# Performance work log

Measured on AMD Instinct MI355X. Metric: run time of the kernel, lower is better.

Reference implementation:

```python
import jax, jax.numpy as jnp
import numpy as np

D_MODEL = 256; N_HEADS = 8; D_FF = 1024; N_LAYERS = 8; N_BLOCKS = 4
VOCAB = 10000; N_SPARSE = 26; N_DENSE = 13; BATCH = 4096
SEQ = N_DENSE + N_SPARSE  # 39 feature tokens


def _ln(x, g, b, eps=1e-5):
    m = jnp.mean(x, -1, keepdims=True)
    v = jnp.mean((x - m) ** 2, -1, keepdims=True)
    return (x - m) * jax.lax.rsqrt(v + eps) * g + b


def _normalize(x, axis=-1, eps=1e-12):
    n = jnp.maximum(jnp.linalg.norm(x, axis=axis, keepdims=True), eps)
    return x / n


def setup_inputs() -> dict:
    key = jax.random.key(0)
    ks = iter(jax.random.split(key, 64))
    d, L, ff = D_MODEL, N_LAYERS, D_FF
    w = lambda shape: jax.random.normal(next(ks), shape, dtype=jnp.float32) * 0.02
    z = lambda shape: jnp.zeros(shape, jnp.float32)
    o = lambda shape: jnp.ones(shape, jnp.float32)
    return {
        "dense_x": jax.random.normal(next(ks), (BATCH, N_DENSE), dtype=jnp.float32),
        "sparse_x": jax.random.randint(next(ks), (BATCH, N_SPARSE), 0, VOCAB, dtype=jnp.int32),
        "W_dense": w((N_DENSE * d, N_DENSE)), "b_dense": z((N_DENSE * d,)),
        "emb": w((N_SPARSE, VOCAB + 1, d)),
        "Wq": w((L, d, d)), "bq": z((L, d)),
        "Wk": w((L, d, d)), "bk": z((L, d)),
        "Wv": w((L, d, d)), "bv": z((L, d)),
        "W1": w((L, ff, d)), "b1": z((L, ff)),
        "W2": w((L, d, ff)), "b2": z((L, d)),
        "n1g": o((L, d)), "n1b": z((L, d)),
        "n2g": o((L, d)), "n2b": z((L, d)),
        "qvec": w((N_BLOCKS, d)),
        "mha_in_w": w((3 * d, d)), "mha_in_b": z((3 * d,)),
        "mha_out_w": w((d, d)), "mha_out_b": z((d,)),
        "ng": o((d,)), "ngb": z((d,)),
        "Wo1": w((D_FF, SEQ * d)), "bo1": z((D_FF,)),
        "Wo2": w((1, D_FF)), "bo2": z((1,)),
    }


def reference(dense_x, sparse_x, W_dense, b_dense, emb, Wq, bq, Wk, bk, Wv, bv,
              W1, b1, W2, b2, n1g, n1b, n2g, n2b, qvec,
              mha_in_w, mha_in_b, mha_out_w, mha_out_b, ng, ngb,
              Wo1, bo1, Wo2, bo2):
    B = dense_x.shape[0]; d = D_MODEL; H = N_HEADS; dh = d // H
    # --- embed_features ---
    dense_emb = (dense_x @ W_dense.T + b_dense).reshape(B, N_DENSE, d)
    emb0 = emb.at[:, 0, :].set(0.0)  # padding_idx=0
    sp = emb0[jnp.arange(N_SPARSE), sparse_x]  # [B, 26, d]
    x = jnp.concatenate([dense_emb, sp], axis=1)  # [B, 39, d]

    scale = 1.0 / jnp.sqrt(jnp.float32(d))  # note: d_model, not head_dim
    block_size = N_LAYERS // N_BLOCKS
    block_outputs = [x]
    for i in range(N_LAYERS):
        # --- HSTU layer: sigmoid pointwise attention ---
        r = x
        h = _ln(x, n1g[i], n1b[i])
        q = (h @ Wq[i].T + bq[i]).reshape(B, SEQ, H, dh).transpose(0, 2, 1, 3)
        k = (h @ Wk[i].T + bk[i]).reshape(B, SEQ, H, dh).transpose(0, 2, 1, 3)
        v = (h @ Wv[i].T + bv[i]).reshape(B, SEQ, H, dh).transpose(0, 2, 1, 3)
        aw = jax.nn.sigmoid(jnp.einsum('bhqd,bhkd->bhqk', q, k) * scale)
        ao = jnp.einsum('bhqk,bhkd->bhqd', aw, v).transpose(0, 2, 1, 3).reshape(B, SEQ, d)
        x = r + ao
        r = x
        h = _ln(x, n2g[i], n2b[i])
        x = r + (jax.nn.relu(h @ W1[i].T + b1[i]) @ W2[i].T + b2[i])
        # --- AttentionResidual block mixing ---
        if (i + 1) % block_size == 0 and i < N_LAYERS - 1:
            V = jnp.stack(block_outputs + [x])  # [n, B, T, d]
            K = _normalize(V)
            qi = min(len(block_outputs), N_BLOCKS - 1)
            qn = _normalize(qvec[qi], axis=0)
            logits = jnp.einsum('d,nbtd->nbt', qn, K)
            wt = jax.nn.softmax(logits, axis=0)
            x = jnp.einsum('nbt,nbtd->btd', wt, V)
            block_outputs.append(x)

    # --- final LayerNorm + standard MHA residual ---
    r = x
    h = _ln(x, ng, ngb)
    qkv = h @ mha_in_w.T + mha_in_b
    q, k, v = jnp.split(qkv, 3, axis=-1)
    q = q.reshape(B, SEQ, H, dh).transpose(0, 2, 1, 3)
    k = k.reshape(B, SEQ, H, dh).transpose(0, 2, 1, 3)
    v = v.reshape(B, SEQ, H, dh).transpose(0, 2, 1, 3)
    at = jax.nn.softmax(jnp.einsum('bhqd,bhkd->bhqk', q, k) / jnp.sqrt(jnp.float32(dh)), axis=-1)
    mo = jnp.einsum('bhqk,bhkd->bhqd', at, v).transpose(0, 2, 1, 3).reshape(B, SEQ, d)
    x = r + (mo @ mha_out_w.T + mha_out_b)

    flat = x.reshape(B, -1)
    return (jax.nn.relu(flat @ Wo1.T + bo1) @ Wo2.T + bo2).squeeze(-1)
```

## Files before the change

kernel.cpp:

```cpp
#include <hip/hip_runtime.h>
#include <hip/hip_bf16.h>

typedef __attribute__((ext_vector_type(4))) float f32x4;
typedef __attribute__((ext_vector_type(8))) short short8;
typedef __attribute__((ext_vector_type(4))) unsigned short us4;

static __device__ __forceinline__ unsigned short f2bf(float f){
  return __builtin_bit_cast(unsigned short, __float2bfloat16(f));
}
static __device__ __forceinline__ float bf2f(unsigned short u){
  return __bfloat162float(__builtin_bit_cast(__hip_bfloat16, u));
}
static __device__ __forceinline__ short8 zero8(){
  short8 v;
#pragma unroll
  for (int e=0;e<8;++e) v[e]=0;
  return v;
}
static __device__ __forceinline__ void g2l16(const void* g, void* l){
  __builtin_amdgcn_global_load_lds(
    (const __attribute__((address_space(1))) unsigned int*)g,
    (__attribute__((address_space(3))) unsigned int*)l, 16, 0, 0);
}

__global__ __launch_bounds__(256)
void qkv_k(const unsigned short* __restrict__ Ap,
           const unsigned short* __restrict__ Bp,
           const float* __restrict__ bias,
           unsigned short* __restrict__ qk,
           unsigned short* __restrict__ vT)
{
  __shared__ __align__(16) unsigned short As[128*256];

  const int tid = threadIdx.x, lane = tid & 63, w = tid >> 6;
  const int cl = lane & 15, q4 = lane >> 4;
  const long rowBase = (long)blockIdx.x << 7;
  const int wm = (w >> 1) << 6, wn = (w & 1) << 6;

#pragma unroll
  for (int it=0; it<16; ++it){
    const int c = (it<<8) + (w<<6) + lane;
    const int kt = c>>10, rem = c & 1023, r = rem>>3, x = rem&7;
    g2l16(Ap + (rowBase + r)*256 + (kt<<6) + (((x ^ (r&7)))<<3),
          As + (((it<<8) + (w<<6))<<3));
  }
  __syncthreads();

  for (int cb=0; cb<6; ++cb){
    f32x4 acc[4][4];
#pragma unroll
    for (int m=0;m<4;++m)
#pragma unroll
      for (int n=0;n<4;++n) acc[m][n] = (f32x4){0.f,0.f,0.f,0.f};
#pragma unroll
    for (int kt=0; kt<4; ++kt)
#pragma unroll
      for (int ks=0; ks<2; ++ks){
        const int kb = ks*64 + (q4<<4);
        short8 af[4], bf_[4];
#pragma unroll
        for (int m=0;m<4;++m){
          const int r = wm + m*16 + cl;
          af[m] = *(const short8*)((const char*)As + (kt<<14) + r*128 + (kb ^ ((r&7)<<4)));
        }
#pragma unroll
        for (int n=0;n<4;++n){
          const long rn = cb*128 + wn + n*16 + cl;
          bf_[n] = *(const short8*)(Bp + rn*256 + (kt<<6) + ks*32 + (q4<<3));
        }
#pragma unroll
        for (int m=0;m<4;++m)
#pragma unroll
          for (int n=0;n<4;++n)
            acc[m][n] = __builtin_amdgcn_mfma_f32_16x16x32_bf16(af[m], bf_[n], acc[m][n], 0,0,0);
      }
#pragma unroll
    for (int n=0;n<4;++n){
      const int col = cb*128 + wn + n*16 + cl;
      const float bi = bias[col];
#pragma unroll
      for (int m=0;m<4;++m){
        const long r0 = rowBase + wm + m*16 + (q4<<2);
#pragma unroll
        for (int i=0;i<4;++i){
          const float v = acc[m][n][i] + bi;
          const long row = r0 + i;
          if (col < 512){
            qk[row*512 + col] = f2bf(v);
          } else {
            const int bb = (int)row / 39;
            const int tt = (int)row - bb*39;
            unsigned short* vrow = vT + ((long)bb*256 + (col - 512))*48;
            vrow[tt] = f2bf(v);
            if (tt < 9) vrow[tt + 39] = 0;
          }
        }
      }
    }
  }
}

__global__ __launch_bounds__(256)
void gemm_k(const unsigned short* __restrict__ Ap, int lda,
            const unsigned short* __restrict__ Bp,
            const float* __restrict__ bias,
            unsigned short* __restrict__ Outp, int ldo, int K, int nColBlk)
{
  const int id = blockIdx.x;
  const int xcd = id & 7; const int t0 = id >> 3;
  const int cb = t0 % nColBlk; const int rb = (t0 / nColBlk)*8 + xcd;
  const long rowBase = (long)rb << 7;
  const long colBase = (long)cb << 7;
  const int tid = threadIdx.x, lane = tid & 63, w = tid >> 6;
  const int wm = (w >> 1) << 6, wn = (w & 1) << 6;
  const int cl = lane & 15, q4 = lane >> 4;

  __shared__ __align__(16) unsigned short As[128*64];
  __shared__ __align__(16) unsigned short Bs[128*64];

  const char* bSrc[4]; unsigned short* bDst[4];
  const char* aSrc[4]; unsigned short* aDst[4];
#pragma unroll
  for (int g=0; g<4; ++g){
    const int c = (w<<8) + (g<<6) + lane;
    const int r = c>>3, x = c&7, c16 = x ^ (r&7);
    bSrc[g] = (const char*)(Bp + (colBase + r)*(long)K) + c16*16;
    bDst[g] = Bs + (((w<<2)+g)<<9);
    aSrc[g] = (const char*)(Ap + (rowBase + r)*(long)lda) + c16*16;
    aDst[g] = As + (((w<<2)+g)<<9);
  }

  f32x4 acc[4][4];
#pragma unroll
  for (int m=0;m<4;++m)
#pragma unroll
    for (int n=0;n<4;++n) acc[m][n] = (f32x4){0.f,0.f,0.f,0.f};

  const int nk = K >> 6;
  for (int t=0; t<nk; ++t){
    if (t) __syncthreads();
    const long tb = (long)t << 7;
#pragma unroll
    for (int g=0; g<4; ++g){
      g2l16(bSrc[g] + tb, bDst[g]);
      g2l16(aSrc[g] + tb, aDst[g]);
    }
    __syncthreads();
#pragma unroll
    for (int ks=0; ks<2; ++ks){
      const int kb = ks*64 + (q4<<4);
      short8 af[4], bf_[4];
#pragma unroll
      for (int m=0;m<4;++m){
        const int r = wm + m*16 + cl;
        af[m] = *(const short8*)((const char*)As + r*128 + (kb ^ ((r&7)<<4)));
      }
#pragma unroll
      for (int n=0;n<4;++n){
        const int r = wn + n*16 + cl;
        bf_[n] = *(const short8*)((const char*)Bs + r*128 + (kb ^ ((r&7)<<4)));
      }
#pragma unroll
      for (int m=0;m<4;++m)
#pragma unroll
        for (int n=0;n<4;++n)
          acc[m][n] = __builtin_amdgcn_mfma_f32_16x16x32_bf16(af[m], bf_[n], acc[m][n], 0,0,0);
    }
  }

#pragma unroll
  for (int n=0;n<4;++n){
    const long col = colBase + wn + n*16 + cl;
    const float bi = bias[col];
#pragma unroll
    for (int m=0;m<4;++m){
      const long r0 = rowBase + wm + m*16 + (q4<<2);
#pragma unroll
      for (int i=0;i<4;++i){
        const float v = acc[m][n][i] + bi;
        Outp[(r0+i)*(long)ldo + col] = f2bf(fmaxf(v,0.f));
      }
    }
  }
}

__global__ __launch_bounds__(256, 2)
void ffn_k(const float* __restrict__ xf_in,
           const float* __restrict__ sB, const float* __restrict__ cB,
           const unsigned short* __restrict__ W1p,
           const float* __restrict__ b1p,
           const unsigned short* __restrict__ W2p,
           const float* __restrict__ b2p,
           float* __restrict__ xf,
           unsigned short* __restrict__ xln1)
{
  __shared__ __align__(16) unsigned short Wb1[64*256];
  __shared__ __align__(16) unsigned short Wb2[256*64];
  __shared__ __align__(16) unsigned short Hs[64*64];
  float* part1 = (float*)Wb1;
  float* part2 = part1 + 256;
  float* sln   = part2 + 256;
  float* cln   = sln + 64;

  const int tid = threadIdx.x, lane = tid & 63, w = tid >> 6;
  const int cl = lane & 15, q4 = lane >> 4;
  const long rowBase = (long)blockIdx.x << 6;

  short8 af[8];
  {
    const int row = (w<<4) + cl;
    const float s = sB[rowBase + row], c = cB[rowBase + row];
    const float* src = xf_in + (rowBase + row)*256 + (q4<<3);
#pragma unroll
    for (int kt=0; kt<8; ++kt){
      f32x4 a = *(const f32x4*)(src + kt*32);
      f32x4 b = *(const f32x4*)(src + kt*32 + 4);
      short8 v;
#pragma unroll
      for (int e=0;e<4;++e){ v[e] = (short)f2bf(a[e]*s + c); v[4+e] = (short)f2bf(b[e]*s + c); }
      af[kt] = v;
    }
  }

  f32x4 acc[4][4];
#pragma unroll
  for (int m=0;m<4;++m)
#pragma unroll
    for (int n=0;n<4;++n) acc[m][n] = (f32x4){0.f,0.f,0.f,0.f};

  for (int j=0; j<16; ++j){
    const int ffbase = j<<6;
    __syncthreads();
#pragma unroll
    for (int it=0; it<8; ++it){
      const int c = (it<<8) + tid;
      {
        const int kt = c>>9, cc = c&511, rr = cc>>3, xs = cc&7;
        g2l16(W1p + ((long)(ffbase+rr))*256 + (kt<<6) + ((xs^(rr&7))<<3),
              Wb1 + (((it<<8) + (w<<6))<<3));
      }
      {
        const int rr = c>>3, xs = c&7;
        g2l16(W2p + (long)rr*1024 + ffbase + ((xs^(rr&7))<<3),
              Wb2 + (((it<<8) + (w<<6))<<3));
      }
    }
    float b1v[4];
#pragma unroll
    for (int n=0;n<4;++n) b1v[n] = b1p[ffbase + n*16 + cl];
    __syncthreads();

    f32x4 hacc[4];
#pragma unroll
    for (int n=0;n<4;++n) hacc[n] = (f32x4){0.f,0.f,0.f,0.f};
#pragma unroll
    for (int kt2=0; kt2<4; ++kt2)
#pragma unroll
      for (int ks=0; ks<2; ++ks){
        const int kb = ks*64 + (q4<<4);
        const short8 a = af[kt2*2 + ks];
#pragma unroll
        for (int n=0;n<4;++n){
          const int rn = n*16 + cl;
          short8 bf_ = *(const short8*)((const char*)Wb1 + (kt2<<13) + rn*128 + (kb ^ ((rn&7)<<4)));
          hacc[n] = __builtin_amdgcn_mfma_f32_16x16x32_bf16(a, bf_, hacc[n], 0,0,0);
        }
      }
#pragma unroll
    for (int n=0;n<4;++n)
#pragma unroll
      for (int i=0;i<4;++i){
        const int hr = (w<<4) + (q4<<2) + i, hc = n*16 + cl;
        const float hv = fmaxf(hacc[n][i] + b1v[n], 0.f);
        *(unsigned short*)((char*)Hs + hr*128 + ((hc*2) ^ ((hr&7)<<4))) = f2bf(hv);
      }
    __syncthreads();

#pragma unroll
    for (int ks=0; ks<2; ++ks){
      const int kb = ks*64 + (q4<<4);
      short8 am[4], bm[4];
#pragma unroll
      for (int m=0;m<4;++m){
        const int r = m*16 + cl;
        am[m] = *(const short8*)((const char*)Hs + r*128 + (kb ^ ((r&7)<<4)));
      }
#pragma unroll
      for (int n=0;n<4;++n){
        const int r = (w<<6) + n*16 + cl;
        bm[n] = *(const short8*)((const char*)Wb2 + r*128 + (kb ^ ((r&7)<<4)));
      }
#pragma unroll
      for (int m=0;m<4;++m)
#pragma unroll
        for (int n=0;n<4;++n)
          acc[m][n] = __builtin_amdgcn_mfma_f32_16x16x32_bf16(am[m], bm[n], acc[m][n], 0,0,0);
    }
  }

#pragma unroll
  for (int n=0;n<4;++n){
    const int col = (w<<6) + n*16 + cl;
    const float bi = b2p[col];
#pragma unroll
    for (int m=0;m<4;++m)
#pragma unroll
      for (int i=0;i<4;++i){
        const int row = m*16 + (q4<<2) + i;
        const long gi = (rowBase + row)*256 + col;
        const float v = acc[m][n][i] + bi + xf[gi];
        acc[m][n][i] = v;
        xf[gi] = v;
      }
  }
  __syncthreads();
#pragma unroll
  for (int m=0;m<4;++m)
#pragma unroll
    for (int i=0;i<4;++i){
      float s1 = 0.f, s2 = 0.f;
#pragma unroll
      for (int n=0;n<4;++n){ const float v = acc[m][n][i]; s1 += v; s2 += v*v; }
#pragma unroll
      for (int off=8; off; off>>=1){ s1 += __shfl_xor(s1, off, 16); s2 += __shfl_xor(s2, off, 16); }
      const int row = m*16 + (q4<<2) + i;
      if (cl == 0){ part1[row*4 + w] = s1; part2[row*4 + w] = s2; }
    }
  __syncthreads();
  if (tid < 64){
    const float S1 = part1[tid*4]+part1[tid*4+1]+part1[tid*4+2]+part1[tid*4+3];
    const float S2 = part2[tid*4]+part2[tid*4+1]+part2[tid*4+2]+part2[tid*4+3];
    const float mn = S1*(1.f/256.f);
    const float var = S2*(1.f/256.f) - mn*mn;
    const float s = rsqrtf(var + 1e-5f);
    sln[tid] = s; cln[tid] = -mn*s;
  }
  __syncthreads();
#pragma unroll
  for (int m=0;m<4;++m)
#pragma unroll
    for (int i=0;i<4;++i){
      const int row = m*16 + (q4<<2) + i;
      const float s = sln[row], c = cln[row];
#pragma unroll
      for (int n=0;n<4;++n){
        const int col = (w<<6) + n*16 + cl;
        xln1[(rowBase + row)*256 + col] = f2bf(acc[m][n][i]*s + c);
      }
    }
}

__global__ __launch_bounds__(256)
void attn_sig_k(const unsigned short* __restrict__ qkb,
                const unsigned short* __restrict__ vT,
                float* xf, float* __restrict__ sB, float* __restrict__ cB)
{
  __shared__ __align__(16) unsigned short Ps[4*48*64];
  __shared__ float part[312];

  const int b = blockIdx.x;
  const int tid = threadIdx.x, lane = tid & 63, w = tid >> 6;
  const int cl = lane & 15, q4 = lane >> 4;
  unsigned short* P = Ps + w*3072;
  const unsigned short* qb = qkb + (long)b*39*512;
  const unsigned short* vbb = vT + (long)b*256*48;

  if (lane < 48){
    const int r = lane;
    *(short8*)((char*)P + r*128 + (96  ^ ((r&7)<<4))) = zero8();
    *(short8*)((char*)P + r*128 + (112 ^ ((r&7)<<4))) = zero8();
  }

  float ps1[3][4], ps2[3][4];
#pragma unroll
  for (int m=0;m<3;++m)
#pragma unroll
    for (int i=0;i<4;++i){ ps1[m][i]=0.f; ps2[m][i]=0.f; }

#pragma unroll
  for (int hh=0; hh<2; ++hh){
    const int h = (w<<1) + hh;
    f32x4 sac[3][3];
#pragma unroll
    for (int m=0;m<3;++m)
#pragma unroll
      for (int n=0;n<3;++n) sac[m][n] = (f32x4){0.f,0.f,0.f,0.f};
    short8 aq[3], bk8[3];
#pragma unroll
    for (int m=0;m<3;++m){
      const int r = m*16 + cl;
      aq[m] = (r < 39) ? *(const short8*)(qb + (long)r*512 + h*32 + q4*8) : zero8();
    }
#pragma unroll
    for (int n=0;n<3;++n){
      const int r = n*16 + cl;
      bk8[n] = (r < 39) ? *(const short8*)(qb + (long)r*512 + 256 + h*32 + q4*8) : zero8();
    }
#pragma unroll
    for (int m=0;m<3;++m)
#pragma unroll
      for (int n=0;n<3;++n)
        sac[m][n] = __builtin_amdgcn_mfma_f32_16x16x32_bf16(aq[m], bk8[n], sac[m][n], 0,0,0);
#pragma unroll
    for (int m=0;m<3;++m)
#pragma unroll
      for (int n=0;n<3;++n)
#pragma unroll
        for (int i=0;i<4;++i){
          const int row = m*16 + (q4<<2) + i, col = n*16 + cl;
          const float pv = 1.f/(1.f + __expf(-sac[m][n][i]*0.0625f));
          *(unsigned short*)((char*)P + row*128 + ((col*2) ^ ((row&7)<<4))) = f2bf(pv);
        }
    f32x4 aoc[3][2];
#pragma unroll
    for (int m=0;m<3;++m)
#pragma unroll
      for (int n=0;n<2;++n) aoc[m][n] = (f32x4){0.f,0.f,0.f,0.f};
#pragma unroll
    for (int ks=0; ks<2; ++ks){
      const int kb = ks*64 + (q4<<4);
      short8 pa[3], vb[2];
#pragma unroll
      for (int m=0;m<3;++m){
        const int r = m*16 + cl;
        pa[m] = *(const short8*)((const char*)P + r*128 + (kb ^ ((r&7)<<4)));
      }
#pragma unroll
      for (int n=0;n<2;++n){
        vb[n] = zero8();
        if (ks == 0 || q4 < 2)
          vb[n] = *(const short8*)(vbb + (long)(h*32 + n*16 + cl)*48 + ks*32 + q4*8);
      }
#pragma unroll
      for (int m=0;m<3;++m)
#pragma unroll
        for (int n=0;n<2;++n)
          aoc[m][n] = __builtin_amdgcn_mfma_f32_16x16x32_bf16(pa[m], vb[n], aoc[m][n], 0,0,0);
    }
#pragma unroll
    for (int m=0;m<3;++m)
#pragma unroll
      for (int n=0;n<2;++n)
#pragma unroll
        for (int i=0;i<4;++i){
          const int row = m*16 + (q4<<2) + i;
          if (row < 39){
            const long gi = (((long)(b*39+row))<<8) + h*32 + n*16 + cl;
            const float nv = xf[gi] + aoc[m][n][i];
            xf[gi] = nv;
            ps1[m][i] += nv; ps2[m][i] += nv*nv;
          }
        }
  }
#pragma unroll
  for (int m=0;m<3;++m)
#pragma unroll
    for (int i=0;i<4;++i){
      float a1 = ps1[m][i], a2 = ps2[m][i];
#pragma unroll
      for (int off=8; off; off>>=1){ a1 += __shfl_xor(a1, off, 16); a2 += __shfl_xor(a2, off, 16); }
      const int row = m*16 + (q4<<2) + i;
      if (cl == 0 && row < 39){ part[row*8 + (w<<1)] = a1; part[row*8 + (w<<1) + 1] = a2; }
    }
  __syncthreads();
  if (tid < 39){
    const float S1 = part[tid*8]+part[tid*8+2]+part[tid*8+4]+part[tid*8+6];
    const float S2 = part[tid*8+1]+part[tid*8+3]+part[tid*8+5]+part[tid*8+7];
    const float mn = S1*(1.f/256.f);
    const float var = S2*(1.f/256.f) - mn*mn;
    const float s = rsqrtf(var + 1e-5f);
    sB[b*39+tid] = s; cB[b*39+tid] = -mn*s;
  }
}

__global__ __launch_bounds__(256)
void attn_fin_k(const unsigned short* __restrict__ qkb,
                const unsigned short* __restrict__ vT,
                const float* __restrict__ xf,
                const unsigned short* __restrict__ moW,
                const float* __restrict__ moB,
                unsigned short* __restrict__ flatb)
{
  __shared__ __align__(16) unsigned short Ps[4*48*64];
  __shared__ __align__(16) unsigned short Mo[48*256];

  const int b = blockIdx.x;
  const int tid = threadIdx.x, lane = tid & 63, w = tid >> 6;
  const int cl = lane & 15, q4 = lane >> 4;
  unsigned short* P = Ps + w*3072;
  const unsigned short* qb = qkb + (long)b*39*512;
  const unsigned short* vbb = vT + (long)b*256*48;
  const float SC = 0.17677669529663687f;

  if (lane < 48){
    const int r = lane;
    *(short8*)((char*)P + r*128 + (96  ^ ((r&7)<<4))) = zero8();
    *(short8*)((char*)P + r*128 + (112 ^ ((r&7)<<4))) = zero8();
  }

#pragma unroll
  for (int hh=0; hh<2; ++hh){
    const int h = (w<<1) + hh;
    f32x4 sac[3][3];
#pragma unroll
    for (int m=0;m<3;++m)
#pragma unroll
      for (int n=0;n<3;++n) sac[m][n] = (f32x4){0.f,0.f,0.f,0.f};
    short8 aq[3], bk8[3];
#pragma unroll
    for (int m=0;m<3;++m){
      const int r = m*16 + cl;
      aq[m] = (r < 39) ? *(const short8*)(qb + (long)r*512 + h*32 + q4*8) : zero8();
    }
#pragma unroll
    for (int n=0;n<3;++n){
      const int r = n*16 + cl;
      bk8[n] = (r < 39) ? *(const short8*)(qb + (long)r*512 + 256 + h*32 + q4*8) : zero8();
    }
#pragma unroll
    for (int m=0;m<3;++m)
#pragma unroll
      for (int n=0;n<3;++n)
        sac[m][n] = __builtin_amdgcn_mfma_f32_16x16x32_bf16(aq[m], bk8[n], sac[m][n], 0,0,0);
#pragma unroll
    for (int m=0;m<3;++m)
#pragma unroll
      for (int i=0;i<4;++i){
        const float v0 = sac[m][0][i]*SC, v1 = sac[m][1][i]*SC, v2 = sac[m][2][i]*SC;
        const bool c2ok = (32 + cl) < 39;
        float mx = fmaxf(v0, v1);
        if (c2ok) mx = fmaxf(mx, v2);
#pragma unroll
        for (int off=8; off; off>>=1) mx = fmaxf(mx, __shfl_xor(mx, off, 16));
        const float e0 = __expf(v0-mx), e1 = __expf(v1-mx);
        const float e2 = c2ok ? __expf(v2-mx) : 0.f;
        float s = e0+e1+e2;
#pragma unroll
        for (int off=8; off; off>>=1) s += __shfl_xor(s, off, 16);
        const float inv = 1.f/s;
        const int row = m*16 + (q4<<2) + i;
        *(unsigned short*)((char*)P + row*128 + (((cl   )*2) ^ ((row&7)<<4))) = f2bf(e0*inv);
        *(unsigned short*)((char*)P + row*128 + (((16+cl)*2) ^ ((row&7)<<4))) = f2bf(e1*inv);
        *(unsigned short*)((char*)P + row*128 + (((32+cl)*2) ^ ((row&7)<<4))) = f2bf(e2*inv);
      }
    f32x4 aoc[3][2];
#pragma unroll
    for (int m=0;m<3;++m)
#pragma unroll
      for (int n=0;n<2;++n) aoc[m][n] = (f32x4){0.f,0.f,0.f,0.f};
#pragma unroll
    for (int ks=0; ks<2; ++ks){
      const int kb = ks*64 + (q4<<4);
      short8 pa[3], vb[2];
#pragma unroll
      for (int m=0;m<3;++m){
        const int r = m*16 + cl;
        pa[m] = *(const short8*)((const char*)P + r*128 + (kb ^ ((r&7)<<4)));
      }
#pragma unroll
      for (int n=0;n<2;++n){
        vb[n] = zero8();
        if (ks == 0 || q4 < 2)
          vb[n] = *(const short8*)(vbb + (long)(h*32 + n*16 + cl)*48 + ks*32 + q4*8);
      }
#pragma unroll
      for (int m=0;m<3;++m)
#pragma unroll
        for (int n=0;n<2;++n)
          aoc[m][n] = __builtin_amdgcn_mfma_f32_16x16x32_bf16(pa[m], vb[n], aoc[m][n], 0,0,0);
    }
#pragma unroll
    for (int m=0;m<3;++m)
#pragma unroll
      for (int n=0;n<2;++n)
#pragma unroll
        for (int i=0;i<4;++i){
          const int row = m*16 + (q4<<2) + i;
          const int colq = h*32 + n*16 + cl;
          *(unsigned short*)((char*)Mo + row*512 + ((colq*2) ^ ((row&7)<<4))) = f2bf(aoc[m][n][i]);
        }
  }
  __syncthreads();
  f32x4 oc[3][4];
#pragma unroll
  for (int m=0;m<3;++m)
#pragma unroll
    for (int n=0;n<4;++n) oc[m][n] = (f32x4){0.f,0.f,0.f,0.f};
#pragma unroll
  for (int ks=0; ks<8; ++ks){
    const int kb = ks*64 + (q4<<4);
    short8 am[3], bm[4];
#pragma unroll
    for (int m=0;m<3;++m){
      const int r = m*16 + cl;
      am[m] = *(const short8*)((const char*)Mo + r*512 + (kb ^ ((r&7)<<4)));
    }
#pragma unroll
    for (int n=0;n<4;++n){
      const int nn = (w<<6) + n*16 + cl;
      bm[n] = *(const short8*)(moW + (long)nn*256 + ks*32 + q4*8);
    }
#pragma unroll
    for (int m=0;m<3;++m)
#pragma unroll
      for (int n=0;n<4;++n)
        oc[m][n] = __builtin_amdgcn_mfma_f32_16x16x32_bf16(am[m], bm[n], oc[m][n], 0,0,0);
  }
#pragma unroll
  for (int m=0;m<3;++m)
#pragma unroll
    for (int n=0;n<4;++n)
#pragma unroll
      for (int i=0;i<4;++i){
        const int row = m*16 + (q4<<2) + i;
        if (row < 39){
          const int col = (w<<6) + n*16 + cl;
          const float v = oc[m][n][i] + moB[col] + xf[(((long)(b*39+row))<<8) + col];
          flatb[(long)b*9984 + row*256 + col] = f2bf(v);
        }
      }
}

__global__ __launch_bounds__(256)
void embed_k(const float* __restrict__ dense_x, const int* __restrict__ sparse_x,
             const float* __restrict__ W_dense, const float* __restrict__ b_dense,
             const float* __restrict__ emb,
             float* __restrict__ xf, unsigned short* __restrict__ x0b,
             unsigned short* __restrict__ xln1)
{
  const int bid = blockIdx.x;
  const int b = bid / 39, t = bid - b*39;
  const int c = threadIdx.x;
  float v;
  if (t < 13){
    const int j = t*256 + c;
    v = b_dense[j];
    const float* wr = W_dense + (long)j*13;
    const float* dx = dense_x + (long)b*13;
#pragma unroll
    for (int k2=0;k2<13;++k2) v = fmaf(dx[k2], wr[k2], v);
  } else {
    const int idx = sparse_x[b*26 + (t-13)];
    v = (idx == 0) ? 0.f : emb[((long)(t-13)*10001 + idx)*256 + c];
  }
  const long row = bid;
  xf[row*256 + c] = v;
  x0b[row*256 + c] = f2bf(v);
  float s1 = v, s2 = v*v;
#pragma unroll
  for (int off=32; off; off>>=1){ s1 += __shfl_xor(s1, off); s2 += __shfl_xor(s2, off); }
  __shared__ float r1[4], r2[4];
  const int lane = c & 63, wq = c >> 6;
  if (lane == 0){ r1[wq]=s1; r2[wq]=s2; }
  __syncthreads();
  const float S1 = r1[0]+r1[1]+r1[2]+r1[3];
  const float S2 = r2[0]+r2[1]+r2[2]+r2[3];
  const float mn = S1*(1.f/256.f);
  const float var = S2*(1.f/256.f) - mn*mn;
  const float s = rsqrtf(var+1e-5f);
  xln1[row*256 + c] = f2bf((v - mn)*s);
}

template<int NSRC>
__global__ __launch_bounds__(256)
void mix_k(float* __restrict__ xf,
           const unsigned short* __restrict__ s0,
           const unsigned short* __restrict__ s1p,
           const unsigned short* __restrict__ s2p,
           unsigned short* mout,
           const float* __restrict__ qvec, int qi,
           unsigned short* __restrict__ xln1)
{
  const int b = blockIdx.x;
  const int tid = threadIdx.x, lane = tid&63, w = tid>>6;
  const int c4 = lane << 2;
  f32x4 q = *(const f32x4*)(qvec + qi*256 + c4);
  float qq = q[0]*q[0]+q[1]*q[1]+q[2]*q[2]+q[3]*q[3];
#pragma unroll
  for (int off=32; off; off>>=1) qq += __shfl_xor(qq, off);
  const float qsc = 1.f/fmaxf(sqrtf(qq), 1e-12f);
#pragma unroll
  for (int e=0;e<4;++e) q[e] *= qsc;
  for (int t = w; t < 39; t += 4){
    const long ro = ((long)(b*39+t))*256 + c4;
    f32x4 v[NSRC];
#pragma unroll
    for (int n=0;n<NSRC;++n){
      if (n == NSRC-1) v[n] = *(const f32x4*)(xf + ro);
      else {
        const unsigned short* sp = (n==0)?s0:((n==1)?s1p:s2p);
        us4 u = *(const us4*)(sp + ro);
#pragma unroll
        for (int e=0;e<4;++e) v[n][e] = bf2f(u[e]);
      }
    }
    float lg[NSRC];
#pragma unroll
    for (int n=0;n<NSRC;++n){
      float nn = v[n][0]*v[n][0]+v[n][1]*v[n][1]+v[n][2]*v[n][2]+v[n][3]*v[n][3];
      float dd = q[0]*v[n][0]+q[1]*v[n][1]+q[2]*v[n][2]+q[3]*v[n][3];
#pragma unroll
      for (int off=32; off; off>>=1){ nn += __shfl_xor(nn,off); dd += __shfl_xor(dd,off); }
      lg[n] = dd / fmaxf(sqrtf(nn), 1e-12f);
    }
    float mx = lg[0];
#pragma unroll
    for (int n=1;n<NSRC;++n) mx = fmaxf(mx, lg[n]);
    float es = 0.f, e_[NSRC];
#pragma unroll
    for (int n=0;n<NSRC;++n){ e_[n] = __expf(lg[n]-mx); es += e_[n]; }
    const float inv = 1.f/es;
    f32x4 o = {0.f,0.f,0.f,0.f};
#pragma unroll
    for (int n=0;n<NSRC;++n){
      const float wt = e_[n]*inv;
#pragma unroll
      for (int e=0;e<4;++e) o[e] = fmaf(wt, v[n][e], o[e]);
    }
    *(f32x4*)(xf + ro) = o;
    if (mout){
      us4 u;
#pragma unroll
      for (int e=0;e<4;++e) u[e] = f2bf(o[e]);
      *(us4*)(mout + ro) = u;
    }
    float s1 = o[0]+o[1]+o[2]+o[3];
    float s2 = o[0]*o[0]+o[1]*o[1]+o[2]*o[2]+o[3]*o[3];
#pragma unroll
    for (int off=32; off; off>>=1){ s1 += __shfl_xor(s1,off); s2 += __shfl_xor(s2,off); }
    const float mn = s1*(1.f/256.f);
    const float var = s2*(1.f/256.f)-mn*mn;
    const float s = rsqrtf(var+1e-5f);
    const float c = -mn*s;
    us4 u2;
#pragma unroll
    for (int e=0;e<4;++e) u2[e] = f2bf(o[e]*s + c);
    *(us4*)(xln1 + ro) = u2;
  }
}

__global__ __launch_bounds__(256)
void head2_k(const unsigned short* __restrict__ h1h, const float* __restrict__ Wo2,
             const float* __restrict__ bo2, float* __restrict__ outp)
{
  const int b = blockIdx.x*4 + (threadIdx.x>>6);
  const int lane = threadIdx.x & 63;
  float s = 0.f;
#pragma unroll
  for (int g=0; g<2; ++g){
    const int base = lane*16 + g*8;
    short8 v8 = *(const short8*)(h1h + (long)b*1024 + base);
#pragma unroll
    for (int e=0;e<8;++e) s = fmaf(bf2f((unsigned short)v8[e]), Wo2[base+e], s);
  }
#pragma unroll
  for (int off=32; off; off>>=1) s += __shfl_xor(s, off);
  if (lane==0) outp[b] = s + bo2[0];
}

__global__ void cvt_k(const float* __restrict__ src, unsigned short* __restrict__ dst, long n){
  const long i = (long)blockIdx.x*256 + threadIdx.x;
  if (i < n) dst[i] = f2bf(src[i]);
}
__global__ void prep_qkv_k(const float* Wq, const float* Wk, const float* Wv,
                           const float* g, unsigned short* dst){
  const int n = blockIdx.x, i = blockIdx.y, k = threadIdx.x;
  const int sel = n >> 8, nn = n & 255;
  const float* W = sel==0?Wq:(sel==1?Wk:Wv);
  dst[((long)i*768 + n)*256 + k] = f2bf(W[((long)i*256+nn)*256 + k] * g[i*256+k]);
}
__global__ void prep_qkvb_k(const float* Wq,const float* Wk,const float* Wv,
                            const float* bq,const float* bk,const float* bv,
                            const float* beta, float* dst){
  const int n = blockIdx.x, i = blockIdx.y, k = threadIdx.x;
  const int sel = n>>8, nn = n&255;
  const float* W = sel==0?Wq:(sel==1?Wk:Wv);
  const float* bb = sel==0?bq:(sel==1?bk:bv);
  float v = beta[i*256+k] * W[((long)i*256+nn)*256+k];
  __shared__ float r[4];
#pragma unroll
  for (int off=32; off; off>>=1) v += __shfl_xor(v, off);
  if ((k&63)==0) r[k>>6] = v;
  __syncthreads();
  if (k==0) dst[i*768+n] = bb[i*256+nn] + r[0]+r[1]+r[2]+r[3];
}
__global__ void prep_w1_k(const float* W1, const float* g, unsigned short* dst){
  const int n = blockIdx.x, i = blockIdx.y, k = threadIdx.x;
  const long o = ((long)i*1024+n)*256 + k;
  dst[o] = f2bf(W1[o] * g[i*256+k]);
}
__global__ void prep_w1b_k(const float* W1, const float* b1, const float* beta, float* dst){
  const int n = blockIdx.x, i = blockIdx.y, k = threadIdx.x;
  float v = beta[i*256+k] * W1[((long)i*1024+n)*256+k];
  __shared__ float r[4];
#pragma unroll
  for (int off=32; off; off>>=1) v += __shfl_xor(v, off);
  if ((k&63)==0) r[k>>6] = v;
  __syncthreads();
  if (k==0) dst[i*1024+n] = b1[i*1024+n] + r[0]+r[1]+r[2]+r[3];
}
__global__ void prep_mha_k(const float* W, const float* g, unsigned short* dst){
  const int n = blockIdx.x, k = threadIdx.x;
  dst[n*256+k] = f2bf(W[n*256+k]*g[k]);
}
__global__ void prep_mhab_k(const float* W, const float* bb, const float* beta, float* dst){
  const int n = blockIdx.x, k = threadIdx.x;
  float v = beta[k]*W[n*256+k];
  __shared__ float r[4];
#pragma unroll
  for (int off=32; off; off>>=1) v += __shfl_xor(v, off);
  if ((k&63)==0) r[k>>6] = v;
  __syncthreads();
  if (k==0) dst[n] = bb[n] + r[0]+r[1]+r[2]+r[3];
}

extern "C" void kernel_launch(void* const* d_in, const int* in_sizes, int n_in,
                              void* d_out, int out_size, void* d_ws, size_t ws_size,
                              hipStream_t stream)
{
  (void)in_sizes; (void)n_in; (void)out_size; (void)ws_size;
  const float* dense_x  = (const float*)d_in[0];
  const int*   sparse_x = (const int*)d_in[1];
  const float* W_dense  = (const float*)d_in[2];
  const float* b_dense  = (const float*)d_in[3];
  const float* emb      = (const float*)d_in[4];
  const float* Wq = (const float*)d_in[5];
  const float* bq = (const float*)d_in[6];
  const float* Wk = (const float*)d_in[7];
  const float* bk = (const float*)d_in[8];
  const float* Wv = (const float*)d_in[9];
  const float* bv = (const float*)d_in[10];
  const float* W1 = (const float*)d_in[11];
  const float* b1 = (const float*)d_in[12];
  const float* W2 = (const float*)d_in[13];
  const float* b2 = (const float*)d_in[14];
  const float* n1g= (const float*)d_in[15];
  const float* n1b= (const float*)d_in[16];
  const float* n2g= (const float*)d_in[17];
  const float* n2b= (const float*)d_in[18];
  const float* qvec=(const float*)d_in[19];
  const float* mha_in_w = (const float*)d_in[20];
  const float* mha_in_b = (const float*)d_in[21];
  const float* mha_out_w= (const float*)d_in[22];
  const float* mha_out_b= (const float*)d_in[23];
  const float* ng = (const float*)d_in[24];
  const float* ngb= (const float*)d_in[25];
  const float* Wo1= (const float*)d_in[26];
  const float* bo1= (const float*)d_in[27];
  const float* Wo2= (const float*)d_in[28];
  const float* bo2= (const float*)d_in[29];

  char* ws = (char*)d_ws;
  size_t off = 0;
  auto alloc = [&](size_t bytes)->void*{ void* p = ws + off; off += (bytes + 255) & ~(size_t)255; return p; };
  float* xf            = (float*)alloc(163577856ull);
  unsigned short* qkh  = (unsigned short*)alloc(163577856ull);
  unsigned short* vT   = (unsigned short*)alloc(100663296ull);
  unsigned short* x0b  = (unsigned short*)alloc(81788928ull);
  unsigned short* m1b  = (unsigned short*)alloc(81788928ull);
  unsigned short* m2b  = (unsigned short*)alloc(81788928ull);
  unsigned short* xln1 = (unsigned short*)alloc(81788928ull);
  unsigned short* h1h  = (unsigned short*)alloc(8388608ull);
  float* sB = (float*)alloc(638976ull);
  float* cB = (float*)alloc(638976ull);
  unsigned short* Wqkv_f = (unsigned short*)alloc(3145728ull);
  float* bqkv_f = (float*)alloc(24576ull);
  unsigned short* W1_f = (unsigned short*)alloc(4194304ull);
  float* b1_f = (float*)alloc(32768ull);
  unsigned short* W2_f = (unsigned short*)alloc(4194304ull);
  unsigned short* mhain_f = (unsigned short*)alloc(393216ull);
  float* mhainb_f = (float*)alloc(3072ull);
  unsigned short* mhaout_f = (unsigned short*)alloc(131072ull);
  unsigned short* Wo1_f = (unsigned short*)alloc(20447232ull);

  unsigned short* flatb = m1b;

  cvt_k<<<8192,256,0,stream>>>(W2, W2_f, 2097152L);
  cvt_k<<<256,256,0,stream>>>(mha_out_w, mhaout_f, 65536L);
  cvt_k<<<39936,256,0,stream>>>(Wo1, Wo1_f, 10223616L);
  prep_qkv_k<<<dim3(768,8),256,0,stream>>>(Wq,Wk,Wv,n1g,Wqkv_f);
  prep_qkvb_k<<<dim3(768,8),256,0,stream>>>(Wq,Wk,Wv,bq,bk,bv,n1b,bqkv_f);
  prep_w1_k<<<dim3(1024,8),256,0,stream>>>(W1,n2g,W1_f);
  prep_w1b_k<<<dim3(1024,8),256,0,stream>>>(W1,b1,n2b,b1_f);
  prep_mha_k<<<768,256,0,stream>>>(mha_in_w, ng, mhain_f);
  prep_mhab_k<<<768,256,0,stream>>>(mha_in_w, mha_in_b, ngb, mhainb_f);

  embed_k<<<159744,256,0,stream>>>(dense_x, sparse_x, W_dense, b_dense, emb, xf, x0b, xln1);

  for (int i = 0; i < 8; ++i){
    qkv_k<<<1248,256,0,stream>>>(xln1, Wqkv_f + (size_t)i*196608, bqkv_f + i*768, qkh, vT);
    attn_sig_k<<<4096,256,0,stream>>>(qkh, vT, xf, sB, cB);
    ffn_k<<<2496,256,0,stream>>>(xf, sB, cB,
        W1_f + (size_t)i*262144, b1_f + i*1024,
        W2_f + (size_t)i*262144, b2 + i*256, xf, xln1);
    if (i == 1)      mix_k<2><<<4096,256,0,stream>>>(xf, x0b, m1b, m2b, m1b, qvec, 1, xln1);
    else if (i == 3) mix_k<3><<<4096,256,0,stream>>>(xf, x0b, m1b, m2b, m2b, qvec, 2, xln1);
    else if (i == 5) mix_k<4><<<4096,256,0,stream>>>(xf, x0b, m1b, m2b, nullptr, qvec, 3, xln1);
  }
  qkv_k<<<1248,256,0,stream>>>(xln1, mhain_f, mhainb_f, qkh, vT);
  attn_fin_k<<<4096,256,0,stream>>>(qkh, vT, xf, mhaout_f, mha_out_b, flatb);
  gemm_k<<<256,256,0,stream>>>(flatb, 9984, Wo1_f, bo1, h1h, 1024, 9984, 8);
  head2_k<<<1024,256,0,stream>>>(h1h, Wo2, bo2, (float*)d_out);
}
```

Baseline: 6.768 ms.

## Double FFN row tile to 128 and skip redundant LN writes before mix

The fused FFN kernel now handles 128 rows per block instead of 64. Each wave computes two 16-row A fragments against the same W1/W2 tiles, so every weight tile staged in shared memory is reused across twice as many rows and weight traffic per row is halved. The grid shrinks from 2496 to 1248 blocks. The accumulator array doubles to 8x4 f32x4, which raises register pressure and may cut occupancy under the 2-waves launch bound. Separately, the LayerNorm bf16 output is no longer written on layers that are followed by the mix kernel, which overwrites it anyway.

```diff
diff --git a/kernel.cpp b/kernel.cpp
--- a/kernel.cpp
+++ b/kernel.cpp
@@ -192,23 +192,24 @@
            const unsigned short* __restrict__ W2p,
            const float* __restrict__ b2p,
            float* __restrict__ xf,
-           unsigned short* __restrict__ xln1)
+           unsigned short* __restrict__ xln1, int writeXln)
 {
   __shared__ __align__(16) unsigned short Wb1[64*256];
   __shared__ __align__(16) unsigned short Wb2[256*64];
-  __shared__ __align__(16) unsigned short Hs[64*64];
+  __shared__ __align__(16) unsigned short Hs[128*64];
   float* part1 = (float*)Wb1;
-  float* part2 = part1 + 256;
-  float* sln   = part2 + 256;
-  float* cln   = sln + 64;
+  float* part2 = part1 + 512;
+  float* sln   = part2 + 512;
+  float* cln   = sln + 128;
 
   const int tid = threadIdx.x, lane = tid & 63, w = tid >> 6;
   const int cl = lane & 15, q4 = lane >> 4;
-  const long rowBase = (long)blockIdx.x << 6;
-
-  short8 af[8];
-  {
-    const int row = (w<<4) + cl;
+  const long rowBase = (long)blockIdx.x << 7;
+
+  short8 af[2][8];
+#pragma unroll
+  for (int p=0; p<2; ++p){
+    const int row = (w<<5) + (p<<4) + cl;
     const float s = sB[rowBase + row], c = cB[rowBase + row];
     const float* src = xf_in + (rowBase + row)*256 + (q4<<3);
 #pragma unroll
@@ -218,13 +219,13 @@
       short8 v;
 #pragma unroll
       for (int e=0;e<4;++e){ v[e] = (short)f2bf(a[e]*s + c); v[4+e] = (short)f2bf(b[e]*s + c); }
-      af[kt] = v;
-    }
-  }
-
-  f32x4 acc[4][4];
-#pragma unroll
-  for (int m=0;m<4;++m)
+      af[p][kt] = v;
+    }
+  }
+
+  f32x4 acc[8][4];
+#pragma unroll
+  for (int m=0;m<8;++m)
 #pragma unroll
     for (int n=0;n<4;++n) acc[m][n] = (f32x4){0.f,0.f,0.f,0.f};
 
@@ -250,51 +251,54 @@
     for (int n=0;n<4;++n) b1v[n] = b1p[ffbase + n*16 + cl];
     __syncthreads();
 
-    f32x4 hacc[4];
-#pragma unroll
-    for (int n=0;n<4;++n) hacc[n] = (f32x4){0.f,0.f,0.f,0.f};
+    f32x4 hacc[2][4];
+#pragma unroll
+    for (int p=0;p<2;++p)
+#pragma unroll
+      for (int n=0;n<4;++n) hacc[p][n] = (f32x4){0.f,0.f,0.f,0.f};
 #pragma unroll
     for (int kt2=0; kt2<4; ++kt2)
 #pragma unroll
       for (int ks=0; ks<2; ++ks){
         const int kb = ks*64 + (q4<<4);
-        const short8 a = af[kt2*2 + ks];
 #pragma unroll
         for (int n=0;n<4;++n){
           const int rn = n*16 + cl;
-          short8 bf_ = *(const short8*)((const char*)Wb1 + (kt2<<13) + rn*128 + (kb ^ ((rn&7)<<4)));
-          hacc[n] = __builtin_amdgcn_mfma_f32_16x16x32_bf16(a, bf_, hacc[n], 0,0,0);
+          const short8 bf_ = *(const short8*)((const char*)Wb1 + (kt2<<13) + rn*128 + (kb ^ ((rn&7)<<4)));
+#pragma unroll
+          for (int p=0;p<2;++p)
+            hacc[p][n] = __builtin_amdgcn_mfma_f32_16x16x32_bf16(af[p][kt2*2+ks], bf_, hacc[p][n], 0,0,0);
         }
       }
 #pragma unroll
-    for (int n=0;n<4;++n)
-#pragma unroll
-      for (int i=0;i<4;++i){
-        const int hr = (w<<4) + (q4<<2) + i, hc = n*16 + cl;
-        const float hv = fmaxf(hacc[n][i] + b1v[n], 0.f);
-        *(unsigned short*)((char*)Hs + hr*128 + ((hc*2) ^ ((hr&7)<<4))) = f2bf(hv);
-      }
+    for (int p=0;p<2;++p)
+#pragma unroll
+      for (int n=0;n<4;++n)
+#pragma unroll
+        for (int i=0;i<4;++i){
+          const int hr = (w<<5) + (p<<4) + (q4<<2) + i, hc = n*16 + cl;
+          const float hv = fmaxf(hacc[p][n][i] + b1v[n], 0.f);
+          *(unsigned short*)((char*)Hs + hr*128 + ((hc*2) ^ ((hr&7)<<4))) = f2bf(hv);
+        }
     __syncthreads();
 
 #pragma unroll
     for (int ks=0; ks<2; ++ks){
       const int kb = ks*64 + (q4<<4);
-      short8 am[4], bm[4];
-#pragma unroll
-      for (int m=0;m<4;++m){
-        const int r = m*16 + cl;
-        am[m] = *(const short8*)((const char*)Hs + r*128 + (kb ^ ((r&7)<<4)));
-      }
+      short8 bm[4];
 #pragma unroll
       for (int n=0;n<4;++n){
         const int r = (w<<6) + n*16 + cl;
         bm[n] = *(const short8*)((const char*)Wb2 + r*128 + (kb ^ ((r&7)<<4)));
       }
 #pragma unroll
-      for (int m=0;m<4;++m)
+      for (int m=0;m<8;++m){
+        const int r = m*16 + cl;
+        const short8 am = *(const short8*)((const char*)Hs + r*128 + (kb ^ ((r&7)<<4)));
 #pragma unroll
         for (int n=0;n<4;++n)
-          acc[m][n] = __builtin_amdgcn_mfma_f32_16x16x32_bf16(am[m], bm[n], acc[m][n], 0,0,0);
+          acc[m][n] = __builtin_amdgcn_mfma_f32_16x16x32_bf16(am, bm[n], acc[m][n], 0,0,0);
+      }
     }
   }
 
@@ -303,7 +307,7 @@
     const int col = (w<<6) + n*16 + cl;
     const float bi = b2p[col];
 #pragma unroll
-    for (int m=0;m<4;++m)
+    for (int m=0;m<8;++m)
 #pragma unroll
       for (int i=0;i<4;++i){
         const int row = m*16 + (q4<<2) + i;
@@ -315,7 +319,7 @@
   }
   __syncthreads();
 #pragma unroll
-  for (int m=0;m<4;++m)
+  for (int m=0;m<8;++m)
 #pragma unroll
     for (int i=0;i<4;++i){
       float s1 = 0.f, s2 = 0.f;
@@ -327,7 +331,7 @@
       if (cl == 0){ part1[row*4 + w] = s1; part2[row*4 + w] = s2; }
     }
   __syncthreads();
-  if (tid < 64){
+  if (tid < 128){
     const float S1 = part1[tid*4]+part1[tid*4+1]+part1[tid*4+2]+part1[tid*4+3];
     const float S2 = part2[tid*4]+part2[tid*4+1]+part2[tid*4+2]+part2[tid*4+3];
     const float mn = S1*(1.f/256.f);
@@ -336,18 +340,20 @@
     sln[tid] = s; cln[tid] = -mn*s;
   }
   __syncthreads();
-#pragma unroll
-  for (int m=0;m<4;++m)
-#pragma unroll
-    for (int i=0;i<4;++i){
-      const int row = m*16 + (q4<<2) + i;
-      const float s = sln[row], c = cln[row];
-#pragma unroll
-      for (int n=0;n<4;++n){
-        const int col = (w<<6) + n*16 + cl;
-        xln1[(rowBase + row)*256 + col] = f2bf(acc[m][n][i]*s + c);
-      }
-    }
+  if (writeXln){
+#pragma unroll
+    for (int m=0;m<8;++m)
+#pragma unroll
+      for (int i=0;i<4;++i){
+        const int row = m*16 + (q4<<2) + i;
+        const float s = sln[row], c = cln[row];
+#pragma unroll
+        for (int n=0;n<4;++n){
+          const int col = (w<<6) + n*16 + cl;
+          xln1[(rowBase + row)*256 + col] = f2bf(acc[m][n][i]*s + c);
+        }
+      }
+  }
 }
 
 __global__ __launch_bounds__(256)
@@ -890,9 +896,10 @@
   for (int i = 0; i < 8; ++i){
     qkv_k<<<1248,256,0,stream>>>(xln1, Wqkv_f + (size_t)i*196608, bqkv_f + i*768, qkh, vT);
     attn_sig_k<<<4096,256,0,stream>>>(qkh, vT, xf, sB, cB);
-    ffn_k<<<2496,256,0,stream>>>(xf, sB, cB,
+    const int wx = (i==1 || i==3 || i==5) ? 0 : 1;
+    ffn_k<<<1248,256,0,stream>>>(xf, sB, cB,
         W1_f + (size_t)i*262144, b1_f + i*1024,
-        W2_f + (size_t)i*262144, b2 + i*256, xf, xln1);
+        W2_f + (size_t)i*262144, b2 + i*256, xf, xln1, wx);
     if (i == 1)      mix_k<2><<<4096,256,0,stream>>>(xf, x0b, m1b, m2b, m1b, qvec, 1, xln1);
     else if (i == 3) mix_k<3><<<4096,256,0,stream>>>(xf, x0b, m1b, m2b, m2b, qvec, 2, xln1);
     else if (i == 5) mix_k<4><<<4096,256,0,stream>>>(xf, x0b, m1b, m2b, nullptr, qvec, 3, xln1);
```

New measurement: 9.454 ms. +39.7%, slower.
